# Performance work log

Hardware: AMD Instinct MI355X
Metric: run time of the kernel (lower is better)

The kernel has to match this reference:

```python
import jax, jax.numpy as jnp
import numpy as np

INPUT_DIM = 128
HIDDEN_DIM = 128
WINDOW_SIZE = 256
BLOCK_SIZE = 256
BATCH = 8
SEQ = 8192


def setup_inputs() -> dict:
    key = jax.random.key(0)
    ks = jax.random.split(key, 7)
    s = 1.0 / np.sqrt(INPUT_DIM)
    return {
        "x": jax.random.normal(ks[0], (BATCH, SEQ, INPUT_DIM), dtype=jnp.float32),
        "Wq": jax.random.normal(ks[1], (HIDDEN_DIM, INPUT_DIM), dtype=jnp.float32) * s,
        "bq": jax.random.normal(ks[2], (HIDDEN_DIM,), dtype=jnp.float32) * s,
        "Wk": jax.random.normal(ks[3], (HIDDEN_DIM, INPUT_DIM), dtype=jnp.float32) * s,
        "bk": jax.random.normal(ks[4], (HIDDEN_DIM,), dtype=jnp.float32) * s,
        "Wv": jax.random.normal(ks[5], (HIDDEN_DIM, INPUT_DIM), dtype=jnp.float32) * s,
        "bv": jax.random.normal(ks[6], (HIDDEN_DIM,), dtype=jnp.float32) * s,
    }


def reference(x, Wq, bq, Wk, bk, Wv, bv):
    B, S, D = x.shape
    bs, w = BLOCK_SIZE, WINDOW_SIZE
    nb = S // bs
    halo = w - 1
    W = bs + 2 * halo  # per-block K/V window width

    q = x @ Wq.T + bq  # [B,S,H]
    k = x @ Wk.T + bk
    v = x @ Wv.T + bv

    # Zero-pad K/V by halo on both sides. Since there is NO softmax, padded
    # zero keys give zero scores and padded zero values contribute zero —
    # this exactly reproduces the torch code's clamped window slicing.
    k_pad = jnp.pad(k, ((0, 0), (halo, halo), (0, 0)))
    v_pad = jnp.pad(v, ((0, 0), (halo, halo), (0, 0)))

    # Gather overlapping windows: [B, nb, W, H]
    starts = jnp.arange(nb) * bs  # window start in padded coords
    idx = starts[:, None] + jnp.arange(W)[None, :]  # [nb, W]
    k_win = k_pad[:, idx, :]
    v_win = v_pad[:, idx, :]

    q_blk = q.reshape(B, nb, bs, -1)  # [B, nb, bs, H]

    scale = 1.0 / jnp.sqrt(jnp.float32(D))
    attn = jnp.einsum('bnqh,bnkh->bnqk', q_blk, k_win) * scale  # no softmax
    out = jnp.einsum('bnqk,bnkh->bnqh', attn, v_win)
    return out.reshape(B, S, -1)
```

## Files before the change

kernel.cpp:

```cpp
#include <hip/hip_runtime.h>
#include <stdint.h>


#define B_ 8
#define S_ 8192

using bf16x8 = __attribute__((ext_vector_type(8))) short;
using s16x4  = __attribute__((ext_vector_type(4))) short;
using f32x16 = __attribute__((ext_vector_type(16))) float;

__device__ __forceinline__ short f2bf(float f) {
  union { float f; uint32_t u; } v; v.f = f;
  uint32_t r = v.u + 0x7fffu + ((v.u >> 16) & 1u);
  return (short)(r >> 16);
}
__device__ __forceinline__ float bf2f(short s) {
  union { uint32_t u; float f; } v; v.u = ((uint32_t)(uint16_t)s) << 16;
  return v.f;
}

#define LDW 136

__global__ __launch_bounds__(256) void proj_kernel(
    const float* __restrict__ x,
    const float* __restrict__ Wq, const float* __restrict__ bq,
    const float* __restrict__ Wk, const float* __restrict__ bk,
    const float* __restrict__ Wv, const float* __restrict__ bv,
    short* __restrict__ qb, short* __restrict__ ktb, short* __restrict__ vtb,
    short* __restrict__ kedge, short* __restrict__ vedge,
    float* __restrict__ Cpart)
{
  __shared__ short wlA[128 * LDW];
  __shared__ short wlB[128 * LDW];

  const int tid  = threadIdx.x;
  const int lane = tid & 63;
  const int wv   = tid >> 6;
  const int c    = lane & 31;
  const int hl   = lane >> 5;
  const int r0   = blockIdx.x * 128;
  const int b    = r0 >> 13;
  const int s0   = r0 & (S_ - 1);

  bf16x8 afrag[8];
  {
    const float* xrow = x + (size_t)(r0 + wv * 32 + c) * 128 + hl * 8;
    #pragma unroll
    for (int kst = 0; kst < 8; ++kst) {
      const float4* p = (const float4*)(xrow + kst * 16);
      float4 f0 = p[0], f1 = p[1];
      bf16x8 a;
      a[0] = f2bf(f0.x); a[1] = f2bf(f0.y); a[2] = f2bf(f0.z); a[3] = f2bf(f0.w);
      a[4] = f2bf(f1.x); a[5] = f2bf(f1.y); a[6] = f2bf(f1.z); a[7] = f2bf(f1.w);
      afrag[kst] = a;
    }
  }

  auto stageW = [&](const float* W, short* wl) {
    #pragma unroll
    for (int it = 0; it < 16; ++it) {
      int l  = it * 256 + tid;
      int n  = l >> 5;
      int k4 = (l & 31) << 2;
      const float4 f = *(const float4*)(W + n * 128 + k4);
      s16x4 o;
      o[0] = f2bf(f.x); o[1] = f2bf(f.y); o[2] = f2bf(f.z); o[3] = f2bf(f.w);
      *(s16x4*)(wl + n * LDW + k4) = o;
    }
  };

  auto gemm = [&](const float* bias, f32x16* acc, const short* wl) {
    #pragma unroll
    for (int nt = 0; nt < 4; ++nt) {
      float bvv = bias[nt * 32 + c];
      #pragma unroll
      for (int i = 0; i < 16; ++i) acc[nt][i] = bvv;
    }
    #pragma unroll
    for (int kst = 0; kst < 8; ++kst) {
      #pragma unroll
      for (int nt = 0; nt < 4; ++nt) {
        bf16x8 bb = *(const bf16x8*)(wl + (nt * 32 + c) * LDW + kst * 16 + hl * 8);
        acc[nt] = __builtin_amdgcn_mfma_f32_32x32x16_bf16(afrag[kst], bb, acc[nt], 0, 0, 0);
      }
    }
  };

  auto writeTransposedLDS = [&](f32x16* acc, short* wl) {
    #pragma unroll
    for (int nt = 0; nt < 4; ++nt) {
      int d = nt * 32 + c;
      #pragma unroll
      for (int g = 0; g < 4; ++g) {
        #pragma unroll
        for (int p = 0; p < 2; ++p) {
          int reg = g * 4 + p * 2;
          int sl  = wv * 32 + g * 8 + hl * 4 + p * 2;
          uint32_t pk = (uint32_t)(uint16_t)f2bf(acc[nt][reg]) |
                        ((uint32_t)(uint16_t)f2bf(acc[nt][reg + 1]) << 16);
          *(uint32_t*)(wl + d * LDW + sl) = pk;
        }
      }
    }
  };

  auto storeTransposed = [&](short* dst, const short* wl) {
    #pragma unroll
    for (int it = 0; it < 8; ++it) {
      int l  = it * 256 + tid;
      int d  = l >> 4;
      int s8 = (l & 15) << 3;
      bf16x8 vv = *(const bf16x8*)(wl + d * LDW + s8);
      *(bf16x8*)(dst + ((size_t)b * 128 + d) * S_ + s0 + s8) = vv;
    }
  };

  auto storeEdge = [&](short* edst, const short* wl) {
    if (tid < 128) {
      size_t eo = ((size_t)b * 32 + (s0 >> 8)) * 256;
      if ((s0 & 255) == 0) edst[eo + tid]       = wl[tid * LDW + 0];
      else                 edst[eo + 128 + tid] = wl[tid * LDW + 127];
    }
  };

  stageW(Wk, wlA);
  __syncthreads();
  {
    f32x16 acc[4];
    gemm(bk, acc, wlA);
    __syncthreads();
    writeTransposedLDS(acc, wlA);
    __syncthreads();
    storeTransposed(ktb, wlA);
    storeEdge(kedge, wlA);
  }

  stageW(Wv, wlB);
  __syncthreads();
  {
    f32x16 acc[4];
    gemm(bv, acc, wlB);
    __syncthreads();
    writeTransposedLDS(acc, wlB);
    __syncthreads();
    storeTransposed(vtb, wlB);
    storeEdge(vedge, wlB);
  }

  {
    f32x16 cacc[4];
    #pragma unroll
    for (int nt = 0; nt < 4; ++nt)
      #pragma unroll
      for (int i = 0; i < 16; ++i) cacc[nt][i] = 0.f;

    #pragma unroll
    for (int kst = 0; kst < 8; ++kst) {
      bf16x8 a = *(const bf16x8*)(wlB + (wv * 32 + c) * LDW + kst * 16 + hl * 8);
      #pragma unroll
      for (int nt = 0; nt < 4; ++nt) {
        bf16x8 bb = *(const bf16x8*)(wlA + (nt * 32 + c) * LDW + kst * 16 + hl * 8);
        cacc[nt] = __builtin_amdgcn_mfma_f32_32x32x16_bf16(a, bb, cacc[nt], 0, 0, 0);
      }
    }

    float* Cp = Cpart + ((size_t)b * 64 + (s0 >> 7)) * 16384;
    #pragma unroll
    for (int nt = 0; nt < 4; ++nt) {
      #pragma unroll
      for (int reg = 0; reg < 16; ++reg) {
        int row = (reg & 3) + 8 * (reg >> 2) + 4 * hl;
        Cp[(wv * 32 + row) * 128 + nt * 32 + c] = cacc[nt][reg];
      }
    }
  }
  __syncthreads();

  stageW(Wq, wlA);
  __syncthreads();
  {
    f32x16 acc[4];
    gemm(bq, acc, wlA);
    __syncthreads();
    #pragma unroll
    for (int nt = 0; nt < 4; ++nt) {
      #pragma unroll
      for (int reg = 0; reg < 16; ++reg) {
        int row = (reg & 3) + 8 * (reg >> 2) + 4 * hl;
        wlA[(wv * 32 + row) * LDW + nt * 32 + c] = f2bf(acc[nt][reg]);
      }
    }
    __syncthreads();
    #pragma unroll
    for (int it = 0; it < 8; ++it) {
      int l  = it * 256 + tid;
      int s  = l >> 4;
      int d8 = (l & 15) << 3;
      bf16x8 vv = *(const bf16x8*)(wlA + s * LDW + d8);
      *(bf16x8*)(qb + (size_t)(r0 + s) * 128 + d8) = vv;
    }
  }
}

#define LDM 136

__global__ __launch_bounds__(512) void attn_kernel(
    const short* __restrict__ qb, const float* __restrict__ Cpart,
    const short* __restrict__ kedge, const short* __restrict__ vedge,
    float* __restrict__ out)
{
  __shared__ __align__(16) short m_l[128 * LDM];
  __shared__ __align__(16) float opat[8 * 32 * 36];

  const int tid  = threadIdx.x;
  const int lane = tid & 63;
  const int wv   = tid >> 6;
  const int c    = lane & 31;
  const int hl   = lane >> 5;
  const int b    = blockIdx.x >> 5;
  const int n    = blockIdx.x & 31;

  float m[32];
  #pragma unroll
  for (int i = 0; i < 32; ++i) m[i] = 0.f;

  const float* Cb0 = Cpart + (size_t)b * 64 * 16384;
  #pragma unroll
  for (int e = 0; e < 6; ++e) {
    int hj = 2 * n - 2 + e;
    if (hj < 0 || hj >= 64) continue;
    const float4* Cp = (const float4*)(Cb0 + (size_t)hj * 16384);
    #pragma unroll
    for (int i4 = 0; i4 < 8; ++i4) {
      float4 f = Cp[i4 * 512 + tid];
      m[i4 * 4 + 0] += f.x; m[i4 * 4 + 1] += f.y;
      m[i4 * 4 + 2] += f.z; m[i4 * 4 + 3] += f.w;
    }
  }

  const int d0 = (tid & 31) << 2;
  if (n > 0) {
    const short* ke = kedge + ((size_t)(b * 32 + n - 1)) * 256;
    const short* ve = vedge + ((size_t)(b * 32 + n - 1)) * 256;
    float k0 = bf2f(ke[d0]),     k1 = bf2f(ke[d0 + 1]);
    float k2 = bf2f(ke[d0 + 2]), k3 = bf2f(ke[d0 + 3]);
    #pragma unroll
    for (int i4 = 0; i4 < 8; ++i4) {
      float vs = bf2f(ve[i4 * 16 + (tid >> 5)]);
      m[i4 * 4 + 0] -= vs * k0; m[i4 * 4 + 1] -= vs * k1;
      m[i4 * 4 + 2] -= vs * k2; m[i4 * 4 + 3] -= vs * k3;
    }
  }
  if (n < 31) {
    const short* ke = kedge + ((size_t)(b * 32 + n + 1)) * 256 + 128;
    const short* ve = vedge + ((size_t)(b * 32 + n + 1)) * 256 + 128;
    float k0 = bf2f(ke[d0]),     k1 = bf2f(ke[d0 + 1]);
    float k2 = bf2f(ke[d0 + 2]), k3 = bf2f(ke[d0 + 3]);
    #pragma unroll
    for (int i4 = 0; i4 < 8; ++i4) {
      float vs = bf2f(ve[i4 * 16 + (tid >> 5)]);
      m[i4 * 4 + 0] -= vs * k0; m[i4 * 4 + 1] -= vs * k1;
      m[i4 * 4 + 2] -= vs * k2; m[i4 * 4 + 3] -= vs * k3;
    }
  }

  const float scale = 0.08838834764831845f;
  #pragma unroll
  for (int i4 = 0; i4 < 8; ++i4) {
    int h = i4 * 16 + (tid >> 5);
    s16x4 o;
    o[0] = f2bf(m[i4 * 4 + 0] * scale); o[1] = f2bf(m[i4 * 4 + 1] * scale);
    o[2] = f2bf(m[i4 * 4 + 2] * scale); o[3] = f2bf(m[i4 * 4 + 3] * scale);
    *(s16x4*)(m_l + h * LDM + d0) = o;
  }

  bf16x8 qf[8];
  {
    const short* q0p = qb + ((size_t)b * S_ + n * 256 + wv * 32 + c) * 128 + hl * 8;
    #pragma unroll
    for (int kst = 0; kst < 8; ++kst) qf[kst] = *(const bf16x8*)(q0p + kst * 16);
  }
  __syncthreads();

  f32x16 oacc[4];
  #pragma unroll
  for (int nt = 0; nt < 4; ++nt)
    #pragma unroll
    for (int i = 0; i < 16; ++i) oacc[nt][i] = 0.f;

  #pragma unroll
  for (int kst = 0; kst < 8; ++kst) {
    #pragma unroll
    for (int nt = 0; nt < 4; ++nt) {
      bf16x8 bb = *(const bf16x8*)(m_l + (nt * 32 + c) * LDM + kst * 16 + hl * 8);
      oacc[nt] = __builtin_amdgcn_mfma_f32_32x32x16_bf16(qf[kst], bb, oacc[nt], 0, 0, 0);
    }
  }

  float* patch = opat + wv * (32 * 36);
  float* outb  = out + ((size_t)b * S_ + n * 256 + wv * 32) * 128;
  #pragma unroll
  for (int nt = 0; nt < 4; ++nt) {
    #pragma unroll
    for (int reg = 0; reg < 16; ++reg) {
      int row = (reg & 3) + 8 * (reg >> 2) + 4 * hl;
      patch[row * 36 + c] = oacc[nt][reg];
    }
    #pragma unroll
    for (int p = 0; p < 4; ++p) {
      int row = p * 8 + (lane >> 3);
      float4 vv = *(const float4*)(patch + row * 36 + (lane & 7) * 4);
      *(float4*)(outb + (size_t)row * 128 + nt * 32 + (lane & 7) * 4) = vv;
    }
  }
}

extern "C" void kernel_launch(void* const* d_in, const int* in_sizes, int n_in,
                              void* d_out, int out_size, void* d_ws, size_t ws_size,
                              hipStream_t stream) {
  const float* x  = (const float*)d_in[0];
  const float* Wq = (const float*)d_in[1];
  const float* bq = (const float*)d_in[2];
  const float* Wk = (const float*)d_in[3];
  const float* bk = (const float*)d_in[4];
  const float* Wv = (const float*)d_in[5];
  const float* bv = (const float*)d_in[6];
  float* out = (float*)d_out;

  const size_t elems = (size_t)B_ * S_ * 128;
  short* qb    = (short*)d_ws;
  short* ktb   = qb + elems;
  short* vtb   = ktb + elems;
  float* Cpart = (float*)(vtb + elems);
  short* kedge = (short*)(Cpart + (size_t)8 * 64 * 16384);
  short* vedge = kedge + (size_t)8 * 32 * 256;

  proj_kernel<<<512, 256, 0, stream>>>(x, Wq, bq, Wk, bk, Wv, bv,
                                       qb, ktb, vtb, kedge, vedge, Cpart);
  attn_kernel<<<256, 512, 0, stream>>>(qb, Cpart, kedge, vedge, out);
}
```

Measured before the change: 129.4 us.

## Split into K/V-summary kernel and fused Q-projection attention kernel, drop dead stores

Removes the unused transposed K/V global stores and the Q intermediate buffer, moving the Q projection into the attention kernel so Q never round-trips through global memory. The K/V kernel now handles 256-row blocks with 512 threads, producing one V^T K partial per block and writing edges from LDS. The attention kernel sums 3 partials instead of 6. x is read twice (once per kernel), and the reuse of LDS between Q and M adds synchronisation.

Result: faster. 120.4 us (-7.0%).

```diff
diff --git a/kernel.cpp b/kernel.cpp
--- a/kernel.cpp
+++ b/kernel.cpp
@@ -4,6 +4,8 @@
 
 #define B_ 8
 #define S_ 8192
+#define LDW 136
+#define LDT 264
 
 using bf16x8 = __attribute__((ext_vector_type(8))) short;
 using s16x4  = __attribute__((ext_vector_type(4))) short;
@@ -19,28 +21,24 @@
   return v.f;
 }
 
-#define LDW 136
-
-__global__ __launch_bounds__(256) void proj_kernel(
+__global__ __launch_bounds__(512) void kv_kernel(
     const float* __restrict__ x,
-    const float* __restrict__ Wq, const float* __restrict__ bq,
     const float* __restrict__ Wk, const float* __restrict__ bk,
     const float* __restrict__ Wv, const float* __restrict__ bv,
-    short* __restrict__ qb, short* __restrict__ ktb, short* __restrict__ vtb,
-    short* __restrict__ kedge, short* __restrict__ vedge,
-    float* __restrict__ Cpart)
+    float* __restrict__ Cpart, short* __restrict__ kedge,
+    short* __restrict__ vedge)
 {
-  __shared__ short wlA[128 * LDW];
-  __shared__ short wlB[128 * LDW];
+  __shared__ short bufK[128 * LDT];
+  __shared__ short bufV[128 * LDT];
 
   const int tid  = threadIdx.x;
   const int lane = tid & 63;
   const int wv   = tid >> 6;
   const int c    = lane & 31;
   const int hl   = lane >> 5;
-  const int r0   = blockIdx.x * 128;
+  const int r0   = blockIdx.x * 256;
   const int b    = r0 >> 13;
-  const int s0   = r0 & (S_ - 1);
+  const int n    = (r0 & (S_ - 1)) >> 8;
 
   bf16x8 afrag[8];
   {
@@ -58,14 +56,14 @@
 
   auto stageW = [&](const float* W, short* wl) {
     #pragma unroll
-    for (int it = 0; it < 16; ++it) {
-      int l  = it * 256 + tid;
-      int n  = l >> 5;
+    for (int it = 0; it < 8; ++it) {
+      int l  = it * 512 + tid;
+      int nn = l >> 5;
       int k4 = (l & 31) << 2;
-      const float4 f = *(const float4*)(W + n * 128 + k4);
+      const float4 f = *(const float4*)(W + nn * 128 + k4);
       s16x4 o;
       o[0] = f2bf(f.x); o[1] = f2bf(f.y); o[2] = f2bf(f.z); o[3] = f2bf(f.w);
-      *(s16x4*)(wl + n * LDW + k4) = o;
+      *(s16x4*)(wl + nn * LDW + k4) = o;
     }
   };
 
@@ -98,138 +96,158 @@
           int sl  = wv * 32 + g * 8 + hl * 4 + p * 2;
           uint32_t pk = (uint32_t)(uint16_t)f2bf(acc[nt][reg]) |
                         ((uint32_t)(uint16_t)f2bf(acc[nt][reg + 1]) << 16);
-          *(uint32_t*)(wl + d * LDW + sl) = pk;
+          *(uint32_t*)(wl + d * LDT + sl) = pk;
         }
       }
     }
   };
 
-  auto storeTransposed = [&](short* dst, const short* wl) {
-    #pragma unroll
-    for (int it = 0; it < 8; ++it) {
-      int l  = it * 256 + tid;
-      int d  = l >> 4;
-      int s8 = (l & 15) << 3;
-      bf16x8 vv = *(const bf16x8*)(wl + d * LDW + s8);
-      *(bf16x8*)(dst + ((size_t)b * 128 + d) * S_ + s0 + s8) = vv;
-    }
-  };
-
-  auto storeEdge = [&](short* edst, const short* wl) {
-    if (tid < 128) {
-      size_t eo = ((size_t)b * 32 + (s0 >> 8)) * 256;
-      if ((s0 & 255) == 0) edst[eo + tid]       = wl[tid * LDW + 0];
-      else                 edst[eo + 128 + tid] = wl[tid * LDW + 127];
-    }
-  };
-
-  stageW(Wk, wlA);
+  stageW(Wk, bufK);
   __syncthreads();
   {
     f32x16 acc[4];
-    gemm(bk, acc, wlA);
+    gemm(bk, acc, bufK);
     __syncthreads();
-    writeTransposedLDS(acc, wlA);
+    writeTransposedLDS(acc, bufK);
+    stageW(Wv, bufV);
+  }
+  __syncthreads();
+
+  {
+    f32x16 acc[4];
+    gemm(bv, acc, bufV);
     __syncthreads();
-    storeTransposed(ktb, wlA);
-    storeEdge(kedge, wlA);
-  }
-
-  stageW(Wv, wlB);
-  __syncthreads();
-  {
-    f32x16 acc[4];
-    gemm(bv, acc, wlB);
-    __syncthreads();
-    writeTransposedLDS(acc, wlB);
-    __syncthreads();
-    storeTransposed(vtb, wlB);
-    storeEdge(vedge, wlB);
-  }
-
-  {
-    f32x16 cacc[4];
-    #pragma unroll
-    for (int nt = 0; nt < 4; ++nt)
-      #pragma unroll
-      for (int i = 0; i < 16; ++i) cacc[nt][i] = 0.f;
-
-    #pragma unroll
-    for (int kst = 0; kst < 8; ++kst) {
-      bf16x8 a = *(const bf16x8*)(wlB + (wv * 32 + c) * LDW + kst * 16 + hl * 8);
-      #pragma unroll
-      for (int nt = 0; nt < 4; ++nt) {
-        bf16x8 bb = *(const bf16x8*)(wlA + (nt * 32 + c) * LDW + kst * 16 + hl * 8);
-        cacc[nt] = __builtin_amdgcn_mfma_f32_32x32x16_bf16(a, bb, cacc[nt], 0, 0, 0);
-      }
-    }
-
-    float* Cp = Cpart + ((size_t)b * 64 + (s0 >> 7)) * 16384;
-    #pragma unroll
-    for (int nt = 0; nt < 4; ++nt) {
+    writeTransposedLDS(acc, bufV);
+  }
+  __syncthreads();
+
+  {
+    const int ht = wv >> 1;
+    const int dh = wv & 1;
+    f32x16 cacc[2];
+    #pragma unroll
+    for (int t = 0; t < 2; ++t)
+      #pragma unroll
+      for (int i = 0; i < 16; ++i) cacc[t][i] = 0.f;
+
+    #pragma unroll
+    for (int kst = 0; kst < 16; ++kst) {
+      bf16x8 a  = *(const bf16x8*)(bufV + (ht * 32 + c) * LDT + kst * 16 + hl * 8);
+      bf16x8 b0 = *(const bf16x8*)(bufK + (dh * 64 + c) * LDT + kst * 16 + hl * 8);
+      bf16x8 b1 = *(const bf16x8*)(bufK + (dh * 64 + 32 + c) * LDT + kst * 16 + hl * 8);
+      cacc[0] = __builtin_amdgcn_mfma_f32_32x32x16_bf16(a, b0, cacc[0], 0, 0, 0);
+      cacc[1] = __builtin_amdgcn_mfma_f32_32x32x16_bf16(a, b1, cacc[1], 0, 0, 0);
+    }
+
+    {
+      size_t eo = ((size_t)(b * 32 + n)) * 256;
+      if (tid < 128)      kedge[eo + tid]               = bufK[tid * LDT + 0];
+      else if (tid < 256) kedge[eo + 128 + (tid - 128)] = bufK[(tid - 128) * LDT + 255];
+      else if (tid < 384) vedge[eo + (tid - 256)]       = bufV[(tid - 256) * LDT + 0];
+      else                vedge[eo + 128 + (tid - 384)] = bufV[(tid - 384) * LDT + 255];
+    }
+
+    float* Cp = Cpart + ((size_t)(b * 32 + n)) * 16384;
+    #pragma unroll
+    for (int t = 0; t < 2; ++t) {
       #pragma unroll
       for (int reg = 0; reg < 16; ++reg) {
         int row = (reg & 3) + 8 * (reg >> 2) + 4 * hl;
-        Cp[(wv * 32 + row) * 128 + nt * 32 + c] = cacc[nt][reg];
+        Cp[(ht * 32 + row) * 128 + dh * 64 + t * 32 + c] = cacc[t][reg];
       }
     }
   }
-  __syncthreads();
-
-  stageW(Wq, wlA);
-  __syncthreads();
-  {
-    f32x16 acc[4];
-    gemm(bq, acc, wlA);
-    __syncthreads();
-    #pragma unroll
-    for (int nt = 0; nt < 4; ++nt) {
-      #pragma unroll
-      for (int reg = 0; reg < 16; ++reg) {
-        int row = (reg & 3) + 8 * (reg >> 2) + 4 * hl;
-        wlA[(wv * 32 + row) * LDW + nt * 32 + c] = f2bf(acc[nt][reg]);
-      }
-    }
-    __syncthreads();
-    #pragma unroll
-    for (int it = 0; it < 8; ++it) {
-      int l  = it * 256 + tid;
-      int s  = l >> 4;
-      int d8 = (l & 15) << 3;
-      bf16x8 vv = *(const bf16x8*)(wlA + s * LDW + d8);
-      *(bf16x8*)(qb + (size_t)(r0 + s) * 128 + d8) = vv;
-    }
-  }
-}
-
-#define LDM 136
-
-__global__ __launch_bounds__(512) void attn_kernel(
-    const short* __restrict__ qb, const float* __restrict__ Cpart,
+}
+
+__global__ __launch_bounds__(512) void qattn_kernel(
+    const float* __restrict__ x,
+    const float* __restrict__ Wq, const float* __restrict__ bq,
+    const float* __restrict__ Cpart,
     const short* __restrict__ kedge, const short* __restrict__ vedge,
     float* __restrict__ out)
 {
-  __shared__ __align__(16) short m_l[128 * LDM];
-  __shared__ __align__(16) float opat[8 * 32 * 36];
+  __shared__ __align__(16) char smem[71680];
+  short* q_l  = (short*)smem;
+  short* m_l  = (short*)smem;
+  float* opat = (float*)(smem + 34816);
 
   const int tid  = threadIdx.x;
   const int lane = tid & 63;
   const int wv   = tid >> 6;
   const int c    = lane & 31;
   const int hl   = lane >> 5;
-  const int b    = blockIdx.x >> 5;
-  const int n    = blockIdx.x & 31;
+  const int r0   = blockIdx.x * 256;
+  const int b    = r0 >> 13;
+  const int n    = (r0 & (S_ - 1)) >> 8;
+
+  bf16x8 afrag[8];
+  {
+    const float* xrow = x + (size_t)(r0 + wv * 32 + c) * 128 + hl * 8;
+    #pragma unroll
+    for (int kst = 0; kst < 8; ++kst) {
+      const float4* p = (const float4*)(xrow + kst * 16);
+      float4 f0 = p[0], f1 = p[1];
+      bf16x8 a;
+      a[0] = f2bf(f0.x); a[1] = f2bf(f0.y); a[2] = f2bf(f0.z); a[3] = f2bf(f0.w);
+      a[4] = f2bf(f1.x); a[5] = f2bf(f1.y); a[6] = f2bf(f1.z); a[7] = f2bf(f1.w);
+      afrag[kst] = a;
+    }
+  }
+
+  #pragma unroll
+  for (int it = 0; it < 8; ++it) {
+    int l  = it * 512 + tid;
+    int nn = l >> 5;
+    int k4 = (l & 31) << 2;
+    const float4 f = *(const float4*)(Wq + nn * 128 + k4);
+    s16x4 o;
+    o[0] = f2bf(f.x); o[1] = f2bf(f.y); o[2] = f2bf(f.z); o[3] = f2bf(f.w);
+    *(s16x4*)(q_l + nn * LDW + k4) = o;
+  }
+  __syncthreads();
+
+  f32x16 qacc[4];
+  #pragma unroll
+  for (int nt = 0; nt < 4; ++nt) {
+    float bvv = bq[nt * 32 + c];
+    #pragma unroll
+    for (int i = 0; i < 16; ++i) qacc[nt][i] = bvv;
+  }
+  #pragma unroll
+  for (int kst = 0; kst < 8; ++kst) {
+    #pragma unroll
+    for (int nt = 0; nt < 4; ++nt) {
+      bf16x8 bb = *(const bf16x8*)(q_l + (nt * 32 + c) * LDW + kst * 16 + hl * 8);
+      qacc[nt] = __builtin_amdgcn_mfma_f32_32x32x16_bf16(afrag[kst], bb, qacc[nt], 0, 0, 0);
+    }
+  }
+  __syncthreads();
+
+  #pragma unroll
+  for (int nt = 0; nt < 4; ++nt) {
+    #pragma unroll
+    for (int reg = 0; reg < 16; ++reg) {
+      int row = (reg & 3) + 8 * (reg >> 2) + 4 * hl;
+      q_l[(wv * 32 + row) * LDW + nt * 32 + c] = f2bf(qacc[nt][reg]);
+    }
+  }
+  __syncthreads();
+
+  bf16x8 qf[8];
+  #pragma unroll
+  for (int kst = 0; kst < 8; ++kst)
+    qf[kst] = *(const bf16x8*)(q_l + (wv * 32 + c) * LDW + kst * 16 + hl * 8);
 
   float m[32];
   #pragma unroll
   for (int i = 0; i < 32; ++i) m[i] = 0.f;
 
-  const float* Cb0 = Cpart + (size_t)b * 64 * 16384;
-  #pragma unroll
-  for (int e = 0; e < 6; ++e) {
-    int hj = 2 * n - 2 + e;
-    if (hj < 0 || hj >= 64) continue;
-    const float4* Cp = (const float4*)(Cb0 + (size_t)hj * 16384);
+  const float* Cb0 = Cpart + (size_t)b * 32 * 16384;
+  #pragma unroll
+  for (int e = 0; e < 3; ++e) {
+    int nn = n - 1 + e;
+    if (nn < 0 || nn > 31) continue;
+    const float4* Cp = (const float4*)(Cb0 + (size_t)nn * 16384);
     #pragma unroll
     for (int i4 = 0; i4 < 8; ++i4) {
       float4 f = Cp[i4 * 512 + tid];
@@ -263,6 +281,7 @@
       m[i4 * 4 + 2] -= vs * k2; m[i4 * 4 + 3] -= vs * k3;
     }
   }
+  __syncthreads();
 
   const float scale = 0.08838834764831845f;
   #pragma unroll
@@ -271,14 +290,7 @@
     s16x4 o;
     o[0] = f2bf(m[i4 * 4 + 0] * scale); o[1] = f2bf(m[i4 * 4 + 1] * scale);
     o[2] = f2bf(m[i4 * 4 + 2] * scale); o[3] = f2bf(m[i4 * 4 + 3] * scale);
-    *(s16x4*)(m_l + h * LDM + d0) = o;
-  }
-
-  bf16x8 qf[8];
-  {
-    const short* q0p = qb + ((size_t)b * S_ + n * 256 + wv * 32 + c) * 128 + hl * 8;
-    #pragma unroll
-    for (int kst = 0; kst < 8; ++kst) qf[kst] = *(const bf16x8*)(q0p + kst * 16);
+    *(s16x4*)(m_l + h * LDW + d0) = o;
   }
   __syncthreads();
 
@@ -292,7 +304,7 @@
   for (int kst = 0; kst < 8; ++kst) {
     #pragma unroll
     for (int nt = 0; nt < 4; ++nt) {
-      bf16x8 bb = *(const bf16x8*)(m_l + (nt * 32 + c) * LDM + kst * 16 + hl * 8);
+      bf16x8 bb = *(const bf16x8*)(m_l + (nt * 32 + c) * LDW + kst * 16 + hl * 8);
       oacc[nt] = __builtin_amdgcn_mfma_f32_32x32x16_bf16(qf[kst], bb, oacc[nt], 0, 0, 0);
     }
   }
@@ -327,15 +339,10 @@
   const float* bv = (const float*)d_in[6];
   float* out = (float*)d_out;
 
-  const size_t elems = (size_t)B_ * S_ * 128;
-  short* qb    = (short*)d_ws;
-  short* ktb   = qb + elems;
-  short* vtb   = ktb + elems;
-  float* Cpart = (float*)(vtb + elems);
-  short* kedge = (short*)(Cpart + (size_t)8 * 64 * 16384);
+  float* Cpart = (float*)d_ws;
+  short* kedge = (short*)(Cpart + (size_t)8 * 32 * 16384);
   short* vedge = kedge + (size_t)8 * 32 * 256;
 
-  proj_kernel<<<512, 256, 0, stream>>>(x, Wq, bq, Wk, bk, Wv, bv,
-                                       qb, ktb, vtb, kedge, vedge, Cpart);
-  attn_kernel<<<256, 512, 0, stream>>>(qb, Cpart, kedge, vedge, out);
-}
+  kv_kernel<<<256, 512, 0, stream>>>(x, Wk, bk, Wv, bv, Cpart, kedge, vedge);
+  qattn_kernel<<<256, 512, 0, stream>>>(x, Wq, bq, Cpart, kedge, vedge, out);
+}
```
